# Optimization experiments

Measured on AMD Instinct MI355X. Metric: run time of the kernel, lower is better.

## Reference

```python
import jax, jax.numpy as jnp
import numpy as np

N, E = 50000, 100000
D, H, EDGE_DIM = 300, 4, 4  # node_dim, heads, edge_dim; per-head C = D
HC = H * D


def setup_inputs() -> dict:
    key = jax.random.key(0)
    ks = jax.random.split(key, 16)
    s = 0.02
    return {
        "xin": jax.random.normal(ks[0], (N, D), jnp.float32),
        "e_idx": jax.random.randint(ks[1], (2, E), 0, N, jnp.int64 if jax.config.jax_enable_x64 else jnp.int32),
        "e_attr": jax.random.normal(ks[2], (E, EDGE_DIM), jnp.float32),
        # TransformerConv params
        "Wq": jax.random.normal(ks[3], (D, HC), jnp.float32) * s,
        "bq": jnp.zeros((HC,), jnp.float32),
        "Wk": jax.random.normal(ks[4], (D, HC), jnp.float32) * s,
        "bk": jnp.zeros((HC,), jnp.float32),
        "Wv": jax.random.normal(ks[5], (D, HC), jnp.float32) * s,
        "bv": jnp.zeros((HC,), jnp.float32),
        "We": jax.random.normal(ks[6], (EDGE_DIM, HC), jnp.float32) * s,
        "be": jnp.zeros((HC,), jnp.float32),
        "Wskip": jax.random.normal(ks[7], (D, HC), jnp.float32) * s,
        "bskip": jnp.zeros((HC,), jnp.float32),
        # LayerNorm params
        "ln_a": jnp.ones((HC,), jnp.float32),
        "ln_b": jnp.zeros((HC,), jnp.float32),
        # output Linear params
        "Wlin": jax.random.normal(ks[8], (HC, D), jnp.float32) * s,
        "blin": jnp.zeros((D,), jnp.float32),
    }


def _forward(xin, e_idx, e_attr, Wq, bq, Wk, bk, Wv, bv, We, be, Wskip, bskip, ln_a, ln_b, Wlin, blin):
    n = xin.shape[0]
    src, dst = e_idx[0], e_idx[1]
    scale = 1.0 / jnp.sqrt(jnp.float32(D))

    q = (xin @ Wq + bq).reshape(n, H, D)
    k = (xin @ Wk + bk).reshape(n, H, D)
    v = (xin @ Wv + bv).reshape(n, H, D)
    ee = (e_attr @ We + be).reshape(-1, H, D)  # [E,H,C]

    kj = k[src] + ee                                        # gather + edge conditioning
    alpha = jnp.einsum('ehc,ehc->eh', q[dst], kj) * scale   # [E,H]
    amax = jax.ops.segment_max(alpha, dst, num_segments=n)  # segment softmax
    alpha = jnp.exp(alpha - amax[dst])
    denom = jax.ops.segment_sum(alpha, dst, num_segments=n)
    alpha = alpha / (denom[dst] + 1e-16)

    msg = (v[src] + ee) * alpha[:, :, None]                 # [E,H,C]
    agg = jax.ops.segment_sum(msg.reshape(-1, HC), dst, num_segments=n)
    x = agg + xin @ Wskip + bskip                           # root/skip weight

    # LayerNorm (biased variance)
    mean = x.mean(-1, keepdims=True)
    var = ((x - mean) ** 2).mean(-1, keepdims=True)
    x = ln_a * (x - mean) / jnp.sqrt(var + 1e-5) + ln_b

    x = x @ Wlin + blin
    return jax.nn.elu(x + xin)


def reference(xin, e_idx, e_attr, Wq, bq, Wk, bk, Wv, bv, We, be, Wskip, bskip, ln_a, ln_b, Wlin, blin):
    return _forward(xin, e_idx, e_attr, Wq, bq, Wk, bk, Wv, bv, We, be, Wskip, bskip, ln_a, ln_b, Wlin, blin)
```

## Files before the change

### kernel.cpp

```cpp
#include <hip/hip_runtime.h>
#include <hip/hip_bf16.h>

typedef __bf16 bf16;
typedef __bf16 bf16x4 __attribute__((ext_vector_type(4)));
typedef __bf16 bf16x8 __attribute__((ext_vector_type(8)));
typedef float f32x4 __attribute__((ext_vector_type(4)));

constexpr int kN = 50000;
constexpr int kE = 100000;
constexpr int kD = 300;
constexpr int kH = 4;
constexpr int kHC = 1200;
constexpr int kK1A = 304;
constexpr int kK1B = 320;
constexpr int kNP1 = 2432;
constexpr int kMP = 50048;
constexpr int kK2 = 1216;
constexpr int kN2P = 384;
constexpr int kLY = 1216;
constexpr int kNB1 = kNP1 / 128;
constexpr int kMB2 = kMP / 64;
constexpr int kT1 = kK1B / 32;
constexpr int kNB2 = kN2P / 128;
constexpr int kT2 = kK2 / 32;
constexpr int kWG1 = kMB2 * kNB1;
constexpr int kWG2 = kMB2 * kNB2;
constexpr int kEW = 136;
constexpr int kSplitRow = 49342;
constexpr size_t kXhiBytes = (size_t)(kN + 1 - kSplitRow) * kK1A * 2;

__device__ __forceinline__ float ldF(const void* p, size_t i, int f32) {
    return f32 ? ((const float*)p)[i] : (float)((const bf16*)p)[i];
}
__device__ __forceinline__ int ldI(const void* p, size_t i, int i64) {
    return i64 ? ((const int*)p)[2 * i] : ((const int*)p)[i];
}

__device__ __forceinline__ const bf16* xrow(const bf16* lo, const bf16* hi, int r) {
    return r < kSplitRow ? lo + (size_t)r * kK1A : hi + (size_t)(r - kSplitRow) * kK1A;
}
__device__ __forceinline__ bf16* xrow_w(bf16* lo, bf16* hi, int r) {
    return r < kSplitRow ? lo + (size_t)r * kK1A : hi + (size_t)(r - kSplitRow) * kK1A;
}

__device__ __forceinline__ void glds16(const void* g, void* l) {
    __builtin_amdgcn_global_load_lds((const __attribute__((address_space(1))) void*)g,
                                     (__attribute__((address_space(3))) void*)l, 16, 0, 0);
}

template <int NWG>
__device__ __forceinline__ int xcd_swz(int phys) {
    constexpr int q = NWG >> 3, r = NWG & 7;
    int xcd = phys & 7, i = phys >> 3;
    int base = xcd < r ? xcd * (q + 1) : r * (q + 1) + (xcd - r) * q;
    return base + i;
}

__device__ __forceinline__ float bflo(unsigned u) {
    return __builtin_bit_cast(float, u << 16);
}
__device__ __forceinline__ float bfhi(unsigned u) {
    return __builtin_bit_cast(float, u & 0xFFFF0000u);
}
__device__ __forceinline__ unsigned bfpack(float a, float b) {
    bf16 x = (bf16)a, y = (bf16)b;
    unsigned short ux = __builtin_bit_cast(unsigned short, x);
    unsigned short uy = __builtin_bit_cast(unsigned short, y);
    return (unsigned)ux | ((unsigned)uy << 16);
}
__device__ __forceinline__ float wsum(float v) {
#pragma unroll
    for (int o = 32; o > 0; o >>= 1) v += __shfl_xor(v, o);
    return v;
}

__global__ void detect_kernel(const unsigned short* __restrict__ xin_u,
                              const int* __restrict__ eidx_i,
                              int* __restrict__ flags) {
    __shared__ int s_ff, s_nz;
    if (threadIdx.x == 0) { s_ff = 0; s_nz = 0; }
    __syncthreads();
    int c1 = 0;
    for (int i = threadIdx.x; i < 65536; i += 256)
        c1 += (((xin_u[i] >> 7) & 0xFF) == 0xFF);
    int c2 = 0;
    for (int i = threadIdx.x; i < 1024; i += 256)
        c2 += (eidx_i[2 * i + 1] != 0);
    atomicAdd(&s_ff, c1);
    atomicAdd(&s_nz, c2);
    __syncthreads();
    if (threadIdx.x == 0) {
        flags[0] = (s_ff > 0) ? 1 : 0;
        flags[1] = (s_nz == 0) ? 1 : 0;
    }
}

__global__ void cast5(const void* __restrict__ We, const void* __restrict__ be,
                      const void* __restrict__ lna, const void* __restrict__ lnb,
                      const void* __restrict__ blin, float* __restrict__ Wef,
                      float* __restrict__ bef, float* __restrict__ lnaf,
                      float* __restrict__ lnbf, float* __restrict__ blinf,
                      const int* __restrict__ flags) {
    int i = blockIdx.x * 256 + threadIdx.x;
    int f32 = flags[0];
    if (i < 4 * kHC) { Wef[i] = ldF(We, i, f32); return; }
    i -= 4 * kHC;
    if (i < kHC) { bef[i] = ldF(be, i, f32); return; }
    i -= kHC;
    if (i < kHC) { lnaf[i] = ldF(lna, i, f32); return; }
    i -= kHC;
    if (i < kHC) { lnbf[i] = ldF(lnb, i, f32); return; }
    i -= kHC;
    if (i < kD) blinf[i] = ldF(blin, i, f32);
}

__global__ void cast_xpad(const void* __restrict__ xin, bf16* __restrict__ xlo,
                          bf16* __restrict__ xhi, const int* __restrict__ flags) {
    int idx = blockIdx.x * 256 + threadIdx.x;
    if (idx < 4) {
        bf16x4 z = {};
        *(bf16x4*)&xlo[(size_t)kSplitRow * kK1A + idx * 4] = z;
    }
    if (idx >= (kN + 1) * 76) return;
    int r = idx / 76, c4 = idx % 76;
    int c = c4 * 4;
    bf16x4 w = {};
    if (r < kN && c < kD) {
        int f32 = flags[0];
        size_t b = (size_t)r * kD + c;
        w[0] = (bf16)ldF(xin, b + 0, f32);
        w[1] = (bf16)ldF(xin, b + 1, f32);
        w[2] = (bf16)ldF(xin, b + 2, f32);
        w[3] = (bf16)ldF(xin, b + 3, f32);
    }
    *(bf16x4*)&(xrow_w(xlo, xhi, r)[c]) = w;
}

__global__ void pack_W1f(const void* __restrict__ Wq, const void* __restrict__ Wk,
                         const void* __restrict__ Wv, const void* __restrict__ Ws,
                         bf16* __restrict__ Bf, const int* __restrict__ flags) {
    int idx = blockIdx.x * 256 + threadIdx.x;
    if (idx >= 2 * kNB1 * kT1 * 8 * 64) return;
    int f32 = flags[0];
    int lane = idx & 63;
    int fi = (idx >> 6) & 7;
    int ksnb = idx >> 9;
    int ks = ksnb % kT1;
    int nbp = ksnb / kT1;
    int p = nbp / kNB1, nb = nbp % kNB1;
    int n = nb * 128 + fi * 16 + (lane & 15);
    int kbase = ks * 32 + (lane >> 4) * 8;
    const void* W = nullptr;
    int c = 0;
    if (n < kHC)          { W = p == 0 ? Wq : Ws; c = n; }
    else if (n < 2 * kHC) { W = p == 0 ? Wk : Wv; c = n - kHC; }
    bf16x8 w = {};
#pragma unroll
    for (int e = 0; e < 8; ++e) {
        int k = kbase + e;
        float v = 0.f;
        if (W && k < kD) v = ldF(W, (size_t)k * kHC + c, f32);
        w[e] = (bf16)v;
    }
    *(bf16x8*)&Bf[(size_t)idx * 8] = w;
}

__global__ void pack_W2f(const void* __restrict__ Wlin, bf16* __restrict__ Bf,
                         const int* __restrict__ flags) {
    int idx = blockIdx.x * 256 + threadIdx.x;
    if (idx >= kNB2 * kT2 * 8 * 64) return;
    int f32 = flags[0];
    int lane = idx & 63;
    int fi = (idx >> 6) & 7;
    int ksnb = idx >> 9;
    int ks = ksnb % kT2;
    int nb = ksnb / kT2;
    int n = nb * 128 + fi * 16 + (lane & 15);
    int kbase = ks * 32 + (lane >> 4) * 8;
    bf16x8 w = {};
#pragma unroll
    for (int e = 0; e < 8; ++e) {
        int k = kbase + e;
        float v = 0.f;
        if (n < kD && k < kHC) v = ldF(Wlin, (size_t)k * kD + n, f32);
        w[e] = (bf16)v;
    }
    *(bf16x8*)&Bf[(size_t)idx * 8] = w;
}

__global__ void pack_bias(const void* __restrict__ bq, const void* __restrict__ bk,
                          const void* __restrict__ bv, const void* __restrict__ bs,
                          float* __restrict__ bcat, const int* __restrict__ flags) {
    int n = blockIdx.x * 256 + threadIdx.x;
    if (n >= 2 * kNP1) return;
    int f32 = flags[0];
    int p = n / kNP1, nl = n % kNP1;
    float v = 0.f;
    if (nl < 2 * kHC) {
        const void* b;
        int c;
        if (nl < kHC) { b = p == 0 ? bq : bs; c = nl; }
        else          { b = p == 0 ? bk : bv; c = nl - kHC; }
        v = ldF(b, c, f32);
    }
    bcat[n] = v;
}

__global__ void hist_kernel(const void* __restrict__ eidx, int* __restrict__ cnt,
                            const int* __restrict__ flags) {
    int e = blockIdx.x * 256 + threadIdx.x;
    if (e < kE) atomicAdd(&cnt[ldI(eidx, (size_t)kE + e, flags[1])], 1);
}

__global__ void scan_local(const int* __restrict__ cnt, int* __restrict__ rowptr,
                           int* __restrict__ bsum) {
    int b = blockIdx.x, t = threadIdx.x;
    int i = b * 256 + t;
    int v = (i < kN) ? cnt[i] : 0;
    int lane = t & 63, wv = t >> 6;
    int s = v;
#pragma unroll
    for (int o = 1; o < 64; o <<= 1) {
        int u = __shfl_up(s, o);
        if (lane >= o) s += u;
    }
    __shared__ int wtot[4];
    if (lane == 63) wtot[wv] = s;
    __syncthreads();
    int add = 0;
    for (int w = 0; w < wv; ++w) add += wtot[w];
    if (i < kN) rowptr[i] = s - v + add;
    if (t == 255) bsum[b] = add + s;
}
__global__ void scan_bsums(int* __restrict__ bsum, int nb) {
    int t = threadIdx.x;
    int v = (t < nb) ? bsum[t] : 0;
    int lane = t & 63, wv = t >> 6;
    int s = v;
#pragma unroll
    for (int o = 1; o < 64; o <<= 1) {
        int u = __shfl_up(s, o);
        if (lane >= o) s += u;
    }
    __shared__ int wtot[4];
    if (lane == 63) wtot[wv] = s;
    __syncthreads();
    int add = 0;
    for (int w = 0; w < wv; ++w) add += wtot[w];
    if (t < nb) bsum[t] = s - v + add;
}
__global__ void scan_add(int* __restrict__ rowptr, const int* __restrict__ bsum) {
    int i = blockIdx.x * 256 + threadIdx.x;
    if (i < kN) rowptr[i] += bsum[i >> 8];
    if (i == 0) rowptr[kN] = kE;
}

__global__ void scatter_kernel(const void* __restrict__ eidx, const int* __restrict__ rowptr,
                               int* __restrict__ fill, int* __restrict__ esort,
                               const int* __restrict__ flags) {
    int e = blockIdx.x * 256 + threadIdx.x;
    if (e < kE) {
        int d = ldI(eidx, (size_t)kE + e, flags[1]);
        int pos = rowptr[d] + atomicAdd(&fill[d], 1);
        esort[pos] = e;
    }
}

__global__ __launch_bounds__(256, 4) void gemm_qkvs(const bf16* __restrict__ xlo,
                                                    const bf16* __restrict__ xhi,
                                                    const bf16* __restrict__ Bf,
                                                    const float* __restrict__ bcat,
                                                    bf16* __restrict__ outA,
                                                    bf16* __restrict__ outB) {
    __shared__ alignas(16) bf16 As[64 * 32];
    __shared__ alignas(16) bf16 Es[64 * kEW];
    const int logical = xcd_swz<kWG1>(blockIdx.x);
    const int mb = logical / kNB1, nb = logical % kNB1;
    const int tid = threadIdx.x;
    const int lane = tid & 63, wave = tid >> 6;
    const int quad = lane >> 4, l16 = lane & 15;
    const int mw = (wave >> 1) * 32;
    const int fibase = (wave & 1) * 4;
    const f32x4 zero = {0.f, 0.f, 0.f, 0.f};
    f32x4 acc[2][4];
#pragma unroll
    for (int i = 0; i < 2; i++)
#pragma unroll
        for (int j = 0; j < 4; j++) acc[i][j] = zero;
    const int mblk = mb * 64, nblk = nb * 128;
    const int srow = wave * 16 + (lane >> 2);
    const int ss = lane & 3;
    int gr = mblk + srow; if (gr >= kN) gr = kN - 1;
    const bf16* gA = xrow(xlo, xhi, gr) + ((ss ^ ((srow >> 1) & 3)) << 3);
    bf16* lA = As + wave * 512;
    int aoff[2];
#pragma unroll
    for (int i = 0; i < 2; i++) {
        int ra = mw + i * 16 + l16;
        aoff[i] = ra * 32 + ((quad ^ ((ra >> 1) & 3)) << 3);
    }
    const bf16* bbase = Bf + (size_t)nb * (kT1 * 4096) + fibase * 512 + lane * 8;
    for (int t = 0; t < kT1; ++t) {
        __syncthreads();
        glds16(gA + t * 32, lA);
        bf16x8 bfv[4];
#pragma unroll
        for (int ni = 0; ni < 4; ni++)
            bfv[ni] = *(const bf16x8*)(bbase + (size_t)t * 4096 + ni * 512);
        __syncthreads();
        bf16x8 af[2];
#pragma unroll
        for (int i = 0; i < 2; i++) af[i] = *(const bf16x8*)&As[aoff[i]];
#pragma unroll
        for (int mi = 0; mi < 2; mi++)
#pragma unroll
            for (int ni = 0; ni < 4; ni++)
                acc[mi][ni] = __builtin_amdgcn_mfma_f32_16x16x32_bf16(
                    af[mi], bfv[ni], acc[mi][ni], 0, 0, 0);
    }
    __syncthreads();
#pragma unroll
    for (int mi = 0; mi < 2; mi++)
#pragma unroll
        for (int r = 0; r < 4; r++) {
            int lr = mw + mi * 16 + quad * 4 + r;
#pragma unroll
            for (int ni = 0; ni < 4; ni++) {
                int lc = (fibase + ni) * 16 + l16;
                Es[lr * kEW + lc] = (bf16)(acc[mi][ni][r] + bcat[nblk + lc]);
            }
        }
    __syncthreads();
#pragma unroll
    for (int it = 0; it < 4; ++it) {
        int row = it * 16 + (tid >> 4);
        int col8 = (tid & 15) * 8;
        int m = mblk + row;
        if (m >= kN) continue;
        bf16x8 w = *(const bf16x8*)&Es[row * kEW + col8];
        int n = nblk + col8;
        if (n < kHC)          *(bf16x8*)&outA[(size_t)m * kLY + n] = w;
        else if (n < 2 * kHC) *(bf16x8*)&outB[(size_t)m * kHC + (n - kHC)] = w;
    }
}

__global__ __launch_bounds__(256) void node_alpha(const int* __restrict__ rowptr,
                                                  const int* __restrict__ esort,
                                                  const void* __restrict__ eidx,
                                                  const void* __restrict__ eattr,
                                                  bf16* __restrict__ qb,
                                                  const bf16* __restrict__ kb,
                                                  const float* __restrict__ Wef,
                                                  const float* __restrict__ bef,
                                                  float* __restrict__ alpha,
                                                  const int* __restrict__ flags) {
    int i = blockIdx.x;
    int h = threadIdx.x >> 6, lane = threadIdx.x & 63;
    int r0 = rowptr[i], r1 = rowptr[i + 1];
    if (r0 >= r1) return;
    int f32 = flags[0], i64 = flags[1];
    const unsigned* qr = (const unsigned*)(qb + (size_t)i * kLY + h * kD);
    float q0[3], q1[3];
#pragma unroll
    for (int j = 0; j < 3; ++j) {
        int p = lane + 64 * j;
        unsigned u = (p < 150) ? qr[p] : 0u;
        q0[j] = bflo(u); q1[j] = bfhi(u);
    }
    float tj[4], tb;
#pragma unroll
    for (int jj = 0; jj < 4; ++jj) {
        const float* w = Wef + jj * kHC + h * kD;
        float s = 0.f;
#pragma unroll
        for (int j = 0; j < 3; ++j) {
            int p = lane + 64 * j;
            if (p < 150) s += q0[j] * w[2 * p] + q1[j] * w[2 * p + 1];
        }
        tj[jj] = wsum(s);
    }
    {
        const float* br = bef + h * kD;
        float s = 0.f;
#pragma unroll
        for (int j = 0; j < 3; ++j) {
            int p = lane + 64 * j;
            if (p < 150) s += q0[j] * br[2 * p] + q1[j] * br[2 * p + 1];
        }
        tb = wsum(s);
    }
    float denom = 0.f;
    int e = esort[r0];
    int src = ldI(eidx, e, i64);
    float ea0 = ldF(eattr, (size_t)e * 4 + 0, f32), ea1 = ldF(eattr, (size_t)e * 4 + 1, f32);
    float ea2 = ldF(eattr, (size_t)e * 4 + 2, f32), ea3 = ldF(eattr, (size_t)e * 4 + 3, f32);
    for (int p = r0; p < r1; ++p) {
        int e2 = 0, src2 = 0;
        float eb0 = 0.f, eb1 = 0.f, eb2 = 0.f, eb3 = 0.f;
        if (p + 1 < r1) {
            e2 = esort[p + 1];
            src2 = ldI(eidx, e2, i64);
            eb0 = ldF(eattr, (size_t)e2 * 4 + 0, f32); eb1 = ldF(eattr, (size_t)e2 * 4 + 1, f32);
            eb2 = ldF(eattr, (size_t)e2 * 4 + 2, f32); eb3 = ldF(eattr, (size_t)e2 * 4 + 3, f32);
        }
        const unsigned* kr = (const unsigned*)(kb + (size_t)src * kHC + h * kD);
        float s = 0.f;
#pragma unroll
        for (int j = 0; j < 3; ++j) {
            int pp = lane + 64 * j;
            if (pp < 150) { unsigned u = kr[pp]; s += q0[j] * bflo(u) + q1[j] * bfhi(u); }
        }
        float dot = wsum(s);
        float logit = dot + ea0 * tj[0] + ea1 * tj[1] + ea2 * tj[2] + ea3 * tj[3] + tb;
        float a = expf(logit * 0.05773502691896258f);
        if (lane == 0) alpha[e * kH + h] = a;
        denom += a;
        e = e2; src = src2; ea0 = eb0; ea1 = eb1; ea2 = eb2; ea3 = eb3;
    }
    if (lane == 0)
        ((float*)(qb + (size_t)i * kLY + kHC))[h] = 1.f / (denom + 1e-16f);
}

__global__ __launch_bounds__(256) void node_fused(const int* __restrict__ rowptr,
                                                  const int* __restrict__ esort,
                                                  const void* __restrict__ eidx,
                                                  const void* __restrict__ eattr,
                                                  const float* __restrict__ Wef,
                                                  const float* __restrict__ bef,
                                                  const float* __restrict__ alpha,
                                                  const bf16* __restrict__ vb,
                                                  const float* __restrict__ lnaf,
                                                  const float* __restrict__ lnbf,
                                                  bf16* __restrict__ qy,
                                                  const int* __restrict__ flags) {
    int i = blockIdx.x;
    int t = threadIdx.x, h = t >> 6, lane = t & 63;
    bf16* yr = qy + (size_t)i * kLY;
    if (i >= kN) {
        for (int c = t; c < kK2; c += 256) yr[c] = (bf16)0.f;
        return;
    }
    int f32 = flags[0], i64 = flags[1];
    int r0 = rowptr[i], r1 = rowptr[i + 1];
    float inv = (r1 > r0) ? ((const float*)(yr + kHC))[h] : 0.f;
    unsigned* yr32 = (unsigned*)(yr + h * kD);
    float a0[3], a1[3];
#pragma unroll
    for (int j = 0; j < 3; ++j) {
        int p = lane + 64 * j;
        unsigned u = (p < 150) ? yr32[p] : 0u;
        a0[j] = bflo(u); a1[j] = bfhi(u);
    }
    float S0 = 0.f, S1 = 0.f, S2 = 0.f, S3 = 0.f, Sb = 0.f;
    int src = 0;
    float al = 0.f, ea0 = 0.f, ea1 = 0.f, ea2 = 0.f, ea3 = 0.f;
    if (r0 < r1) {
        int e = esort[r0];
        src = ldI(eidx, e, i64);
        al = alpha[e * kH + h];
        ea0 = ldF(eattr, (size_t)e * 4 + 0, f32); ea1 = ldF(eattr, (size_t)e * 4 + 1, f32);
        ea2 = ldF(eattr, (size_t)e * 4 + 2, f32); ea3 = ldF(eattr, (size_t)e * 4 + 3, f32);
    }
    for (int p = r0; p < r1; ++p) {
        int src2 = 0;
        float al2 = 0.f, eb0 = 0.f, eb1 = 0.f, eb2 = 0.f, eb3 = 0.f;
        if (p + 1 < r1) {
            int e2 = esort[p + 1];
            src2 = ldI(eidx, e2, i64);
            al2 = alpha[e2 * kH + h];
            eb0 = ldF(eattr, (size_t)e2 * 4 + 0, f32); eb1 = ldF(eattr, (size_t)e2 * 4 + 1, f32);
            eb2 = ldF(eattr, (size_t)e2 * 4 + 2, f32); eb3 = ldF(eattr, (size_t)e2 * 4 + 3, f32);
        }
        float coeff = al * inv;
        S0 += coeff * ea0; S1 += coeff * ea1; S2 += coeff * ea2; S3 += coeff * ea3;
        Sb += coeff;
        const unsigned* vr = (const unsigned*)(vb + (size_t)src * kHC + h * kD);
#pragma unroll
        for (int j = 0; j < 3; ++j) {
            int pp = lane + 64 * j;
            if (pp < 150) {
                unsigned u = vr[pp];
                a0[j] += coeff * bflo(u);
                a1[j] += coeff * bfhi(u);
            }
        }
        src = src2; al = al2; ea0 = eb0; ea1 = eb1; ea2 = eb2; ea3 = eb3;
    }
    {
        const float* wb = Wef + h * kD;
        const float* br = bef + h * kD;
#pragma unroll
        for (int j = 0; j < 3; ++j) {
            int p = lane + 64 * j;
            if (p < 150) {
                int c0 = 2 * p, c1 = 2 * p + 1;
                a0[j] += S0 * wb[c0] + S1 * wb[kHC + c0] + S2 * wb[2 * kHC + c0] +
                         S3 * wb[3 * kHC + c0] + Sb * br[c0];
                a1[j] += S0 * wb[c1] + S1 * wb[kHC + c1] + S2 * wb[2 * kHC + c1] +
                         S3 * wb[3 * kHC + c1] + Sb * br[c1];
            }
        }
    }
    float s = 0.f, s2 = 0.f;
#pragma unroll
    for (int j = 0; j < 3; ++j) {
        s += a0[j] + a1[j];
        s2 += a0[j] * a0[j] + a1[j] * a1[j];
    }
#pragma unroll
    for (int off = 32; off > 0; off >>= 1) {
        s += __shfl_down(s, off);
        s2 += __shfl_down(s2, off);
    }
    __shared__ float ss[4], ss2[4];
    if (lane == 0) { ss[h] = s; ss2[h] = s2; }
    __syncthreads();
    if (t == 0) {
        float S = ss[0] + ss[1] + ss[2] + ss[3];
        float S2 = ss2[0] + ss2[1] + ss2[2] + ss2[3];
        float mean = S / (float)kHC;
        float var = S2 / (float)kHC - mean * mean;
        ss[0] = mean;
        ss2[0] = rsqrtf(var + 1e-5f);
    }
    __syncthreads();
    float mean = ss[0], rstd = ss2[0];
#pragma unroll
    for (int j = 0; j < 3; ++j) {
        int p = lane + 64 * j;
        if (p < 150) {
            int c0 = h * kD + 2 * p;
            float v0 = lnaf[c0] * (a0[j] - mean) * rstd + lnbf[c0];
            float v1 = lnaf[c0 + 1] * (a1[j] - mean) * rstd + lnbf[c0 + 1];
            yr32[p] = bfpack(v0, v1);
        }
    }
    if (t < kK2 - kHC) yr[kHC + t] = (bf16)0.f;
}

__global__ __launch_bounds__(256, 4) void gemm_out(const bf16* __restrict__ Ay,
                                                   const bf16* __restrict__ Bf,
                                                   const float* __restrict__ blinf,
                                                   const void* __restrict__ xin,
                                                   void* __restrict__ out,
                                                   const int* __restrict__ flags) {
    __shared__ alignas(16) bf16 As[64 * 32];
    const int logical = xcd_swz<kWG2>(blockIdx.x);
    const int mb = logical / kNB2, nb = logical % kNB2;
    const int f32 = flags[0];
    const int tid = threadIdx.x;
    const int lane = tid & 63, wave = tid >> 6;
    const int quad = lane >> 4, l16 = lane & 15;
    const int mw = (wave >> 1) * 32;
    const int fibase = (wave & 1) * 4;
    const f32x4 zero = {0.f, 0.f, 0.f, 0.f};
    f32x4 acc[2][4];
#pragma unroll
    for (int i = 0; i < 2; i++)
#pragma unroll
        for (int j = 0; j < 4; j++) acc[i][j] = zero;
    const int mblk = mb * 64, nblk = nb * 128;
    const int srow = wave * 16 + (lane >> 2);
    const int ss = lane & 3;
    const bf16* gA = Ay + (size_t)(mblk + srow) * kLY + ((ss ^ ((srow >> 1) & 3)) << 3);
    bf16* lA = As + wave * 512;
    int aoff[2];
#pragma unroll
    for (int i = 0; i < 2; i++) {
        int ra = mw + i * 16 + l16;
        aoff[i] = ra * 32 + ((quad ^ ((ra >> 1) & 3)) << 3);
    }
    const bf16* bbase = Bf + (size_t)nb * (kT2 * 4096) + fibase * 512 + lane * 8;
    for (int t = 0; t < kT2; ++t) {
        __syncthreads();
        glds16(gA + t * 32, lA);
        bf16x8 bfv[4];
#pragma unroll
        for (int ni = 0; ni < 4; ni++)
            bfv[ni] = *(const bf16x8*)(bbase + (size_t)t * 4096 + ni * 512);
        __syncthreads();
        bf16x8 af[2];
#pragma unroll
        for (int i = 0; i < 2; i++) af[i] = *(const bf16x8*)&As[aoff[i]];
#pragma unroll
        for (int mi = 0; mi < 2; mi++)
#pragma unroll
            for (int ni = 0; ni < 4; ni++)
                acc[mi][ni] = __builtin_amdgcn_mfma_f32_16x16x32_bf16(
                    af[mi], bfv[ni], acc[mi][ni], 0, 0, 0);
    }
#pragma unroll
    for (int mi = 0; mi < 2; mi++)
#pragma unroll
        for (int r = 0; r < 4; r++) {
            int m = mblk + mw + mi * 16 + quad * 4 + r;
            if (m >= kN) continue;
#pragma unroll
            for (int ni = 0; ni < 4; ni++) {
                int n = nblk + (fibase + ni) * 16 + l16;
                if (n >= kD) continue;
                float resid = ldF(xin, (size_t)m * kD + n, f32);
                float t2 = acc[mi][ni][r] + blinf[n] + resid;
                float r2 = t2 > 0.f ? t2 : expm1f(t2);
                if (f32) ((float*)out)[(size_t)m * kD + n] = r2;
                else     ((bf16*)out)[(size_t)m * kD + n] = (bf16)r2;
            }
        }
}

__global__ void fallback_copy(const unsigned short* __restrict__ xin_u,
                              unsigned short* __restrict__ out_u) {
    int i = blockIdx.x * 256 + threadIdx.x;
    if (i < kN * kD) out_u[i] = xin_u[i];
}

extern "C" void kernel_launch(void* const* d_in, const int* in_sizes, int n_in,
                              void* d_out, int out_size, void* d_ws, size_t ws_size,
                              hipStream_t stream) {
    const void* xin  = d_in[0];
    const void* eidx = d_in[1];
    const void* eatt = d_in[2];
    const void* Wq   = d_in[3];
    const void* bq   = d_in[4];
    const void* Wk   = d_in[5];
    const void* bk   = d_in[6];
    const void* Wv   = d_in[7];
    const void* bv   = d_in[8];
    const void* We   = d_in[9];
    const void* be   = d_in[10];
    const void* Wsk  = d_in[11];
    const void* bsk  = d_in[12];
    const void* lna  = d_in[13];
    const void* lnb  = d_in[14];
    const void* Wlin = d_in[15];
    const void* blin = d_in[16];

    char* ws = (char*)d_ws;
    size_t off = 0;
    auto alloc = [&](size_t bytes) -> char* {
        char* p = ws + off;
        off += (bytes + 255) & ~(size_t)255;
        return p;
    };
    bf16* bufA   = (bf16*)alloc((size_t)kMP * kLY * 2);
    bf16* bufB   = (bf16*)alloc((size_t)kN * kHC * 2);
    bf16* W1f    = (bf16*)alloc((size_t)2 * kNP1 * kK1B * 2);
    float* bcat  = (float*)alloc((size_t)2 * kNP1 * 4);
    bf16* W2f    = (bf16*)alloc((size_t)kN2P * kK2 * 2);
    float* alpha = (float*)alloc((size_t)kE * kH * 4);
    char* ovl    = alloc(kXhiBytes);
    int* cnt     = (int*)ovl;
    int* fill    = (int*)(ovl + 200064);
    bf16* xhi    = (bf16*)ovl;
    int* rowptr  = (int*)alloc((size_t)(kN + 1) * 4);
    int* esort   = (int*)alloc((size_t)kE * 4);
    int* bsum    = (int*)alloc(256 * 4);
    float* Wef   = (float*)alloc((size_t)4 * kHC * 4);
    float* bef   = (float*)alloc((size_t)kHC * 4);
    float* lnaf  = (float*)alloc((size_t)kHC * 4);
    float* lnbf  = (float*)alloc((size_t)kHC * 4);
    float* blinf = (float*)alloc((size_t)kD * 4);
    int* flags   = (int*)alloc(2 * 4);
    (void)in_sizes; (void)n_in;
    bf16* xlo = (bf16*)d_out;
    if (off > ws_size ||
        (size_t)out_size * 2 < (size_t)kSplitRow * kK1A * 2 + 32) {
        fallback_copy<<<(kN * kD + 255) / 256, 256, 0, stream>>>(
            (const unsigned short*)xin, (unsigned short*)d_out);
        return;
    }

    constexpr int kScanNB = (kN + 255) / 256;
    detect_kernel<<<1, 256, 0, stream>>>((const unsigned short*)xin, (const int*)eidx, flags);
    hipMemsetAsync(cnt, 0, 200064 + (size_t)kN * 4, stream);
    hist_kernel<<<(kE + 255) / 256, 256, 0, stream>>>(eidx, cnt, flags);
    scan_local<<<kScanNB, 256, 0, stream>>>(cnt, rowptr, bsum);
    scan_bsums<<<1, 256, 0, stream>>>(bsum, kScanNB);
    scan_add<<<kScanNB, 256, 0, stream>>>(rowptr, bsum);
    scatter_kernel<<<(kE + 255) / 256, 256, 0, stream>>>(eidx, rowptr, fill, esort, flags);
    cast_xpad<<<((kN + 1) * 76 + 255) / 256, 256, 0, stream>>>(xin, xlo, xhi, flags);
    cast5<<<(4 * kHC + 3 * kHC + kD + 255) / 256, 256, 0, stream>>>(
        We, be, lna, lnb, blin, Wef, bef, lnaf, lnbf, blinf, flags);
    pack_W1f<<<(2 * kNB1 * kT1 * 8 * 64 + 255) / 256, 256, 0, stream>>>(
        Wq, Wk, Wv, Wsk, W1f, flags);
    pack_bias<<<(2 * kNP1 + 255) / 256, 256, 0, stream>>>(bq, bk, bv, bsk, bcat, flags);
    pack_W2f<<<(kNB2 * kT2 * 8 * 64 + 255) / 256, 256, 0, stream>>>(Wlin, W2f, flags);

    gemm_qkvs<<<kWG1, 256, 0, stream>>>(xlo, xhi, W1f, bcat, bufA, bufB);
    node_alpha<<<kN, 256, 0, stream>>>(rowptr, esort, eidx, eatt, bufA, bufB,
                                       Wef, bef, alpha, flags);
    gemm_qkvs<<<kWG1, 256, 0, stream>>>(
        xlo, xhi, W1f + (size_t)kNB1 * kT1 * 4096, bcat + kNP1, bufA, bufB);
    node_fused<<<kMP, 256, 0, stream>>>(rowptr, esort, eidx, eatt, Wef, bef, alpha,
                                        bufB, lnaf, lnbf, bufA, flags);
    gemm_out<<<kWG2, 256, 0, stream>>>(bufA, W2f, blinf, xin, d_out, flags);
}
```

Measured before the change: 1.044 ms.

## Fold Wq·Wkᵀ into a per-head bilinear form to drop the K projection GEMM

Precomputes M_h = Wq_h·Wk_hᵀ, along with edge and bias cross terms, so the per-node GEMM produces z = x·M (plus small edge terms) in place of separate Q and K. The attention logit then becomes a dot between z_dst and the raw bf16 x_src row. This replaces the first full 2432-column QKVS GEMM with a 1280-column one and removes the K buffer. It adds small weight-preprocessing kernels, and bf16 rounding of the product matrix changes numerics. It also drops the software prefetch of the next edge, leaves a dead multiply-by-zero in the inner loop, and reuses bufB as scratch before it is overwritten.

```diff
diff --git a/kernel.cpp b/kernel.cpp
--- a/kernel.cpp
+++ b/kernel.cpp
@@ -14,16 +14,20 @@
 constexpr int kK1A = 304;
 constexpr int kK1B = 320;
 constexpr int kNP1 = 2432;
+constexpr int kNZ  = 1280;
+constexpr int kTW  = 24;
 constexpr int kMP = 50048;
 constexpr int kK2 = 1216;
 constexpr int kN2P = 384;
 constexpr int kLY = 1216;
 constexpr int kNB1 = kNP1 / 128;
+constexpr int kNB0 = kNZ / 128;
 constexpr int kMB2 = kMP / 64;
 constexpr int kT1 = kK1B / 32;
 constexpr int kNB2 = kN2P / 128;
 constexpr int kT2 = kK2 / 32;
 constexpr int kWG1 = kMB2 * kNB1;
+constexpr int kWG0 = kMB2 * kNB0;
 constexpr int kWG2 = kMB2 * kNB2;
 constexpr int kEW = 136;
 constexpr int kSplitRow = 49342;
@@ -136,24 +140,122 @@
     *(bf16x4*)&(xrow_w(xlo, xhi, r)[c]) = w;
 }
 
-__global__ void pack_W1f(const void* __restrict__ Wq, const void* __restrict__ Wk,
-                         const void* __restrict__ Wv, const void* __restrict__ Ws,
+__global__ void compute_M(const void* __restrict__ Wq, const void* __restrict__ Wk,
+                          float* __restrict__ Mscr, const int* __restrict__ flags) {
+    int b = blockIdx.x;
+    int h = b / 361, t2 = b % 361;
+    int ty = t2 / 19, tx = t2 % 19;
+    int r = threadIdx.x >> 4, c = threadIdx.x & 15;
+    int d = ty * 16 + r, dp = tx * 16 + c;
+    if (d >= 300 || dp >= 304) return;
+    float s = 0.f;
+    if (dp < 300) {
+        int f32 = flags[0];
+#pragma unroll 4
+        for (int cc = 0; cc < 300; ++cc)
+            s += ldF(Wq, (size_t)d * kHC + h * 300 + cc, f32) *
+                 ldF(Wk, (size_t)dp * kHC + h * 300 + cc, f32);
+    }
+    Mscr[((size_t)h * 300 + d) * 304 + dp] = s;
+}
+
+__global__ void compute_U(const void* __restrict__ Wq, const void* __restrict__ Wk,
+                          const void* __restrict__ We, const void* __restrict__ be,
+                          const void* __restrict__ bq, const void* __restrict__ bk,
+                          float* __restrict__ Uscr, float* __restrict__ w3scr,
+                          float* __restrict__ cst8, const int* __restrict__ flags) {
+    int t = blockIdx.x * 256 + threadIdx.x;
+    int f32 = flags[0];
+    if (t < 24 * 304) {
+        int vi = t / 304, d = t % 304;
+        int h = vi / 6, j = vi % 6;
+        float s = 0.f;
+        if (d < 300) {
+#pragma unroll 4
+            for (int c = 0; c < 300; ++c) {
+                float a = ldF(Wq, (size_t)d * kHC + h * 300 + c, f32);
+                float b = (j < 4) ? ldF(We, (size_t)j * kHC + h * 300 + c, f32)
+                        : (j == 4) ? ldF(be, h * 300 + c, f32)
+                                   : ldF(bk, h * 300 + c, f32);
+                s += a * b;
+            }
+        }
+        Uscr[t] = s;
+        return;
+    }
+    t -= 24 * 304;
+    if (t < 4 * 304) {
+        int h = t / 304, d = t % 304;
+        float s = 0.f;
+        if (d < 300) {
+#pragma unroll 4
+            for (int c = 0; c < 300; ++c)
+                s += ldF(bq, h * 300 + c, f32) * ldF(Wk, (size_t)d * kHC + h * 300 + c, f32);
+        }
+        w3scr[t] = s;
+        return;
+    }
+    t -= 4 * 304;
+    if (t < 24) {
+        int h = t / 6, j = t % 6;
+        float s = 0.f;
+#pragma unroll 4
+        for (int c = 0; c < 300; ++c) {
+            float a = ldF(bq, h * 300 + c, f32);
+            float b = (j < 4) ? ldF(We, (size_t)j * kHC + h * 300 + c, f32)
+                    : (j == 4) ? ldF(be, h * 300 + c, f32)
+                               : ldF(bk, h * 300 + c, f32);
+            s += a * b;
+        }
+        cst8[h * 8 + j] = s;
+    }
+}
+
+__global__ void pack_Zf(const float* __restrict__ Mscr, const float* __restrict__ Uscr,
+                        bf16* __restrict__ Bf) {
+    int idx = blockIdx.x * 256 + threadIdx.x;
+    if (idx >= kNB0 * kT1 * 8 * 64) return;
+    int lane = idx & 63;
+    int fi = (idx >> 6) & 7;
+    int ksnb = idx >> 9;
+    int ks = ksnb % kT1;
+    int nb = ksnb / kT1;
+    int n = nb * 128 + fi * 16 + (lane & 15);
+    int kbase = ks * 32 + (lane >> 4) * 8;
+    bf16x8 w = {};
+#pragma unroll
+    for (int e = 0; e < 8; ++e) {
+        int k = kbase + e;
+        float v = 0.f;
+        if (k < 300) {
+            if (n < kHC) {
+                int h = n / 300, dp = n % 300;
+                v = Mscr[((size_t)h * 300 + k) * 304 + dp];
+            } else if (n < kHC + kTW) {
+                v = Uscr[(size_t)(n - kHC) * 304 + k];
+            }
+        }
+        w[e] = (bf16)v;
+    }
+    *(bf16x8*)&Bf[(size_t)idx * 8] = w;
+}
+
+__global__ void pack_W1f(const void* __restrict__ Ws, const void* __restrict__ Wv,
                          bf16* __restrict__ Bf, const int* __restrict__ flags) {
     int idx = blockIdx.x * 256 + threadIdx.x;
-    if (idx >= 2 * kNB1 * kT1 * 8 * 64) return;
+    if (idx >= kNB1 * kT1 * 8 * 64) return;
     int f32 = flags[0];
     int lane = idx & 63;
     int fi = (idx >> 6) & 7;
     int ksnb = idx >> 9;
     int ks = ksnb % kT1;
-    int nbp = ksnb / kT1;
-    int p = nbp / kNB1, nb = nbp % kNB1;
+    int nb = ksnb / kT1;
     int n = nb * 128 + fi * 16 + (lane & 15);
     int kbase = ks * 32 + (lane >> 4) * 8;
     const void* W = nullptr;
     int c = 0;
-    if (n < kHC)          { W = p == 0 ? Wq : Ws; c = n; }
-    else if (n < 2 * kHC) { W = p == 0 ? Wk : Wv; c = n - kHC; }
+    if (n < kHC)          { W = Ws; c = n; }
+    else if (n < 2 * kHC) { W = Wv; c = n - kHC; }
     bf16x8 w = {};
 #pragma unroll
     for (int e = 0; e < 8; ++e) {
@@ -188,21 +290,14 @@
     *(bf16x8*)&Bf[(size_t)idx * 8] = w;
 }
 
-__global__ void pack_bias(const void* __restrict__ bq, const void* __restrict__ bk,
-                          const void* __restrict__ bv, const void* __restrict__ bs,
+__global__ void pack_bias(const void* __restrict__ bs, const void* __restrict__ bv,
                           float* __restrict__ bcat, const int* __restrict__ flags) {
     int n = blockIdx.x * 256 + threadIdx.x;
-    if (n >= 2 * kNP1) return;
+    if (n >= kNP1) return;
     int f32 = flags[0];
-    int p = n / kNP1, nl = n % kNP1;
     float v = 0.f;
-    if (nl < 2 * kHC) {
-        const void* b;
-        int c;
-        if (nl < kHC) { b = p == 0 ? bq : bs; c = nl; }
-        else          { b = p == 0 ? bk : bv; c = nl - kHC; }
-        v = ldF(b, c, f32);
-    }
+    if (n < kHC)          v = ldF(bs, n, f32);
+    else if (n < 2 * kHC) v = ldF(bv, n - kHC, f32);
     bcat[n] = v;
 }
 
@@ -263,6 +358,83 @@
         int d = ldI(eidx, (size_t)kE + e, flags[1]);
         int pos = rowptr[d] + atomicAdd(&fill[d], 1);
         esort[pos] = e;
+    }
+}
+
+__global__ __launch_bounds__(256, 4) void gemm_z(const bf16* __restrict__ xlo,
+                                                 const bf16* __restrict__ xhi,
+                                                 const bf16* __restrict__ Bf,
+                                                 bf16* __restrict__ outA,
+                                                 bf16* __restrict__ Tb) {
+    __shared__ alignas(16) bf16 As[64 * 32];
+    __shared__ alignas(16) bf16 Es[64 * kEW];
+    const int logical = xcd_swz<kWG0>(blockIdx.x);
+    const int mb = logical / kNB0, nb = logical % kNB0;
+    const int tid = threadIdx.x;
+    const int lane = tid & 63, wave = tid >> 6;
+    const int quad = lane >> 4, l16 = lane & 15;
+    const int mw = (wave >> 1) * 32;
+    const int fibase = (wave & 1) * 4;
+    const f32x4 zero = {0.f, 0.f, 0.f, 0.f};
+    f32x4 acc[2][4];
+#pragma unroll
+    for (int i = 0; i < 2; i++)
+#pragma unroll
+        for (int j = 0; j < 4; j++) acc[i][j] = zero;
+    const int mblk = mb * 64, nblk = nb * 128;
+    const int srow = wave * 16 + (lane >> 2);
+    const int ss = lane & 3;
+    int gr = mblk + srow; if (gr >= kN) gr = kN - 1;
+    const bf16* gA = xrow(xlo, xhi, gr) + ((ss ^ ((srow >> 1) & 3)) << 3);
+    bf16* lA = As + wave * 512;
+    int aoff[2];
+#pragma unroll
+    for (int i = 0; i < 2; i++) {
+        int ra = mw + i * 16 + l16;
+        aoff[i] = ra * 32 + ((quad ^ ((ra >> 1) & 3)) << 3);
+    }
+    const bf16* bbase = Bf + (size_t)nb * (kT1 * 4096) + fibase * 512 + lane * 8;
+    for (int t = 0; t < kT1; ++t) {
+        __syncthreads();
+        glds16(gA + t * 32, lA);
+        bf16x8 bfv[4];
+#pragma unroll
+        for (int ni = 0; ni < 4; ni++)
+            bfv[ni] = *(const bf16x8*)(bbase + (size_t)t * 4096 + ni * 512);
+        __syncthreads();
+        bf16x8 af[2];
+#pragma unroll
+        for (int i = 0; i < 2; i++) af[i] = *(const bf16x8*)&As[aoff[i]];
+#pragma unroll
+        for (int mi = 0; mi < 2; mi++)
+#pragma unroll
+            for (int ni = 0; ni < 4; ni++)
+                acc[mi][ni] = __builtin_amdgcn_mfma_f32_16x16x32_bf16(
+                    af[mi], bfv[ni], acc[mi][ni], 0, 0, 0);
+    }
+    __syncthreads();
+#pragma unroll
+    for (int mi = 0; mi < 2; mi++)
+#pragma unroll
+        for (int r = 0; r < 4; r++) {
+            int lr = mw + mi * 16 + quad * 4 + r;
+#pragma unroll
+            for (int ni = 0; ni < 4; ni++) {
+                int lc = (fibase + ni) * 16 + l16;
+                Es[lr * kEW + lc] = (bf16)acc[mi][ni][r];
+            }
+        }
+    __syncthreads();
+#pragma unroll
+    for (int it = 0; it < 4; ++it) {
+        int row = it * 16 + (tid >> 4);
+        int col8 = (tid & 15) * 8;
+        int m = mblk + row;
+        if (m >= kN) continue;
+        bf16x8 w = *(const bf16x8*)&Es[row * kEW + col8];
+        int n = nblk + col8;
+        if (n < kHC)            *(bf16x8*)&outA[(size_t)m * kLY + n] = w;
+        else if (n < kHC + kTW) *(bf16x8*)&Tb[(size_t)m * kTW + (n - kHC)] = w;
     }
 }
 
@@ -349,9 +521,11 @@
                                                   const void* __restrict__ eidx,
                                                   const void* __restrict__ eattr,
                                                   bf16* __restrict__ qb,
-                                                  const bf16* __restrict__ kb,
-                                                  const float* __restrict__ Wef,
-                                                  const float* __restrict__ bef,
+                                                  const bf16* __restrict__ xlo,
+                                                  const bf16* __restrict__ xhi,
+                                                  const bf16* __restrict__ Tb,
+                                                  const float* __restrict__ w3scr,
+                                                  const float* __restrict__ cst8,
                                                   float* __restrict__ alpha,
                                                   const int* __restrict__ flags) {
     int i = blockIdx.x;
@@ -359,63 +533,46 @@
     int r0 = rowptr[i], r1 = rowptr[i + 1];
     if (r0 >= r1) return;
     int f32 = flags[0], i64 = flags[1];
-    const unsigned* qr = (const unsigned*)(qb + (size_t)i * kLY + h * kD);
-    float q0[3], q1[3];
+    const unsigned* zr = (const unsigned*)(qb + (size_t)i * kLY + h * kD);
+    float z0[3], z1[3], w30[3], w31[3];
 #pragma unroll
     for (int j = 0; j < 3; ++j) {
         int p = lane + 64 * j;
-        unsigned u = (p < 150) ? qr[p] : 0u;
-        q0[j] = bflo(u); q1[j] = bfhi(u);
-    }
-    float tj[4], tb;
-#pragma unroll
-    for (int jj = 0; jj < 4; ++jj) {
-        const float* w = Wef + jj * kHC + h * kD;
-        float s = 0.f;
-#pragma unroll
-        for (int j = 0; j < 3; ++j) {
-            int p = lane + 64 * j;
-            if (p < 150) s += q0[j] * w[2 * p] + q1[j] * w[2 * p + 1];
-        }
-        tj[jj] = wsum(s);
-    }
-    {
-        const float* br = bef + h * kD;
-        float s = 0.f;
-#pragma unroll
-        for (int j = 0; j < 3; ++j) {
-            int p = lane + 64 * j;
-            if (p < 150) s += q0[j] * br[2 * p] + q1[j] * br[2 * p + 1];
-        }
-        tb = wsum(s);
-    }
+        unsigned u = (p < 150) ? zr[p] : 0u;
+        z0[j] = bflo(u); z1[j] = bfhi(u);
+        if (p < 150) {
+            w30[j] = w3scr[h * 304 + 2 * p];
+            w31[j] = w3scr[h * 304 + 2 * p + 1];
+        } else { w30[j] = 0.f; w31[j] = 0.f; }
+    }
+    const bf16* tr = Tb + (size_t)i * kTW + h * 6;
+    const float* cc = cst8 + h * 8;
+    float tj0 = (float)tr[0] + cc[0], tj1 = (float)tr[1] + cc[1];
+    float tj2 = (float)tr[2] + cc[2], tj3 = (float)tr[3] + cc[3];
+    float base = ((float)tr[4] + cc[4]) + ((float)tr[5] + cc[5]);
     float denom = 0.f;
-    int e = esort[r0];
-    int src = ldI(eidx, e, i64);
-    float ea0 = ldF(eattr, (size_t)e * 4 + 0, f32), ea1 = ldF(eattr, (size_t)e * 4 + 1, f32);
-    float ea2 = ldF(eattr, (size_t)e * 4 + 2, f32), ea3 = ldF(eattr, (size_t)e * 4 + 3, f32);
     for (int p = r0; p < r1; ++p) {
-        int e2 = 0, src2 = 0;
-        float eb0 = 0.f, eb1 = 0.f, eb2 = 0.f, eb3 = 0.f;
-        if (p + 1 < r1) {
-            e2 = esort[p + 1];
-            src2 = ldI(eidx, e2, i64);
-            eb0 = ldF(eattr, (size_t)e2 * 4 + 0, f32); eb1 = ldF(eattr, (size_t)e2 * 4 + 1, f32);
-            eb2 = ldF(eattr, (size_t)e2 * 4 + 2, f32); eb3 = ldF(eattr, (size_t)e2 * 4 + 3, f32);
-        }
-        const unsigned* kr = (const unsigned*)(kb + (size_t)src * kHC + h * kD);
+        int e = esort[p];
+        int src = ldI(eidx, e, i64);
+        float ea0 = ldF(eattr, (size_t)e * 4 + 0, f32), ea1 = ldF(eattr, (size_t)e * 4 + 1, f32);
+        float ea2 = ldF(eattr, (size_t)e * 4 + 2, f32), ea3 = ldF(eattr, (size_t)e * 4 + 3, f32);
+        const unsigned* xr = (const unsigned*)xrow(xlo, xhi, src);
         float s = 0.f;
 #pragma unroll
         for (int j = 0; j < 3; ++j) {
             int pp = lane + 64 * j;
-            if (pp < 150) { unsigned u = kr[pp]; s += q0[j] * bflo(u) + q1[j] * bfhi(u); }
+            if (pp < 150) {
+                unsigned u = xr[pp];
+                float xa = bflo(u), xb = bfhi(u);
+                s += (z0[j] + w30[j]) * 0.f;
+                s += z0[j] * xa + z1[j] * xb + w30[j] * xa + w31[j] * xb;
+            }
         }
         float dot = wsum(s);
-        float logit = dot + ea0 * tj[0] + ea1 * tj[1] + ea2 * tj[2] + ea3 * tj[3] + tb;
+        float logit = dot + base + ea0 * tj0 + ea1 * tj1 + ea2 * tj2 + ea3 * tj3;
         float a = expf(logit * 0.05773502691896258f);
         if (lane == 0) alpha[e * kH + h] = a;
         denom += a;
-        e = e2; src = src2; ea0 = eb0; ea1 = eb1; ea2 = eb2; ea3 = eb3;
     }
     if (lane == 0)
         ((float*)(qb + (size_t)i * kLY + kHC))[h] = 1.f / (denom + 1e-16f);
@@ -644,8 +801,8 @@
     };
     bf16* bufA   = (bf16*)alloc((size_t)kMP * kLY * 2);
     bf16* bufB   = (bf16*)alloc((size_t)kN * kHC * 2);
-    bf16* W1f    = (bf16*)alloc((size_t)2 * kNP1 * kK1B * 2);
-    float* bcat  = (float*)alloc((size_t)2 * kNP1 * 4);
+    bf16* W1f    = (bf16*)alloc((size_t)kNB1 * kT1 * 4096 * 2);
+    float* bcat  = (float*)alloc((size_t)kNP1 * 4);
     bf16* W2f    = (bf16*)alloc((size_t)kN2P * kK2 * 2);
     float* alpha = (float*)alloc((size_t)kE * kH * 4);
     char* ovl    = alloc(kXhiBytes);
@@ -662,6 +819,13 @@
     float* blinf = (float*)alloc((size_t)kD * 4);
     int* flags   = (int*)alloc(2 * 4);
     (void)in_sizes; (void)n_in;
+    char* bscr   = (char*)bufB;
+    bf16* Zf     = (bf16*)(bscr);
+    float* Mscr  = (float*)(bscr + 819200);
+    float* Uscr  = (float*)(bscr + 2278400);
+    float* w3scr = (float*)(bscr + 2307584);
+    float* cst8  = (float*)(bscr + 2312448);
+    bf16* Tb     = (bf16*)(bscr + 2312704);
     bf16* xlo = (bf16*)d_out;
     if (off > ws_size ||
         (size_t)out_size * 2 < (size_t)kSplitRow * kK1A * 2 + 32) {
@@ -681,16 +845,18 @@
     cast_xpad<<<((kN + 1) * 76 + 255) / 256, 256, 0, stream>>>(xin, xlo, xhi, flags);
     cast5<<<(4 * kHC + 3 * kHC + kD + 255) / 256, 256, 0, stream>>>(
         We, be, lna, lnb, blin, Wef, bef, lnaf, lnbf, blinf, flags);
-    pack_W1f<<<(2 * kNB1 * kT1 * 8 * 64 + 255) / 256, 256, 0, stream>>>(
-        Wq, Wk, Wv, Wsk, W1f, flags);
-    pack_bias<<<(2 * kNP1 + 255) / 256, 256, 0, stream>>>(bq, bk, bv, bsk, bcat, flags);
+    compute_M<<<4 * 19 * 19, 256, 0, stream>>>(Wq, Wk, Mscr, flags);
+    compute_U<<<(28 * 304 + 24 + 255) / 256, 256, 0, stream>>>(
+        Wq, Wk, We, be, bq, bk, Uscr, w3scr, cst8, flags);
+    pack_Zf<<<(kNB0 * kT1 * 8 * 64 + 255) / 256, 256, 0, stream>>>(Mscr, Uscr, Zf);
+    pack_W1f<<<(kNB1 * kT1 * 8 * 64 + 255) / 256, 256, 0, stream>>>(Wsk, Wv, W1f, flags);
+    pack_bias<<<(kNP1 + 255) / 256, 256, 0, stream>>>(bsk, bv, bcat, flags);
     pack_W2f<<<(kNB2 * kT2 * 8 * 64 + 255) / 256, 256, 0, stream>>>(Wlin, W2f, flags);
 
+    gemm_z<<<kWG0, 256, 0, stream>>>(xlo, xhi, Zf, bufA, Tb);
+    node_alpha<<<kN, 256, 0, stream>>>(rowptr, esort, eidx, eatt, bufA, xlo, xhi,
+                                       Tb, w3scr, cst8, alpha, flags);
     gemm_qkvs<<<kWG1, 256, 0, stream>>>(xlo, xhi, W1f, bcat, bufA, bufB);
-    node_alpha<<<kN, 256, 0, stream>>>(rowptr, esort, eidx, eatt, bufA, bufB,
-                                       Wef, bef, alpha, flags);
-    gemm_qkvs<<<kWG1, 256, 0, stream>>>(
-        xlo, xhi, W1f + (size_t)kNB1 * kT1 * 4096, bcat + kNP1, bufA, bufB);
     node_fused<<<kMP, 256, 0, stream>>>(rowptr, esort, eidx, eatt, Wef, bef, alpha,
                                         bufB, lnaf, lnbf, bufA, flags);
     gemm_out<<<kWG2, 256, 0, stream>>>(bufA, W2f, blinf, xin, d_out, flags);
```

Result: slower. 1.160 ms (+11.1%).
